# Optimization experiments

Measured on AMD Instinct MI355X. Metric: run time of the kernel, lower is better.

Reference implementation:

```python
import jax, jax.numpy as jnp
import numpy as np

EPS = 1e-5

def conv2d(x, w, b, stride, pad):
    y = jax.lax.conv_general_dilated(x, w, (stride, stride), [(pad, pad), (pad, pad)],
                                     dimension_numbers=('NCHW', 'OIHW', 'NCHW'))
    return y + b[None, :, None, None]

def group_norm(x, w, b, groups=8):
    B, C, H, W = x.shape
    xg = x.reshape(B, groups, C // groups, H, W)
    mu = xg.mean(axis=(2, 3, 4), keepdims=True)
    var = xg.var(axis=(2, 3, 4), keepdims=True)
    xn = ((xg - mu) / jnp.sqrt(var + EPS)).reshape(B, C, H, W)
    return xn * w[None, :, None, None] + b[None, :, None, None]

def _apply_1q(state, gate, wire):
    # state: (N,2,2,2,2), gate: (N,2,2) or (2,2); wire axis = wire+1
    ax = wire + 1
    st = jnp.moveaxis(state, ax, -1)
    if gate.ndim == 3:
        st = jnp.einsum('nij,n...j->n...i', gate, st)
    else:
        st = jnp.einsum('ij,n...j->n...i', gate, st)
    return jnp.moveaxis(st, -1, ax)

def _cnot(state, c, t):
    axc, axt = c + 1, t + 1
    s0 = jnp.take(state, 0, axis=axc)
    s1 = jnp.take(state, 1, axis=axc)
    axt2 = axt - 1 if axt > axc else axt
    s1 = jnp.flip(s1, axis=axt2)
    return jnp.stack([s0, s1], axis=axc)

def quanv_circuit(patches, weights):
    # patches: (N,4) angles; weights: (4,3) Rot params. Returns (N,4) <Z_i>.
    N = patches.shape[0]
    state = jnp.zeros((N, 2, 2, 2, 2), jnp.complex64).at[:, 0, 0, 0, 0].set(1.0)
    for w in range(4):
        a = patches[:, w] * 0.5
        ca, sa = jnp.cos(a), jnp.sin(a)
        # RX(angle): AngleEmbedding default rotation='X'
        rx = jnp.stack([jnp.stack([ca + 0j, -1j * sa], -1),
                        jnp.stack([-1j * sa, ca + 0j], -1)], -2)  # (N,2,2)
        phi, theta, omega = weights[w, 0], weights[w, 1], weights[w, 2]
        ct, st = jnp.cos(theta * 0.5), jnp.sin(theta * 0.5)
        # Rot(phi,theta,omega) = RZ(omega) RY(theta) RZ(phi)
        rot = jnp.stack([
            jnp.stack([jnp.exp(-1j * (phi + omega) * 0.5) * ct,
                       -jnp.exp(1j * (phi - omega) * 0.5) * st]),
            jnp.stack([jnp.exp(-1j * (phi - omega) * 0.5) * st,
                       jnp.exp(1j * (phi + omega) * 0.5) * ct])]).astype(jnp.complex64)
        gate = jnp.einsum('ij,njk->nik', rot, rx)  # fuse Rot o RX
        state = _apply_1q(state, gate, w)
    for c in range(3):
        state = _cnot(state, c, c + 1)
    probs = state.real ** 2 + state.imag ** 2  # (N,2,2,2,2)
    ez = []
    for w in range(4):
        other = tuple(ax for ax in range(1, 5) if ax != w + 1)
        p = probs.sum(axis=other)  # (N,2)
        ez.append(p[:, 0] - p[:, 1])
    return jnp.stack(ez, -1)

def _forward(x, pre_w1, pre_b1, pre_w2, pre_b2, pre_w3, pre_b3, qweights,
             conv1_w, conv1_b, gn1_w, gn1_b, conv2_w, conv2_b, gn2_w, gn2_b,
             fc1_w, fc1_b, fc2_w, fc2_b):
    h = jax.nn.relu(conv2d(x, pre_w1, pre_b1, 2, 1))
    h = jax.nn.relu(conv2d(h, pre_w2, pre_b2, 2, 1))
    h = conv2d(h, pre_w3, pre_b3, 1, 0)  # (B,4,14,14)
    B, C, H, W = h.shape
    oh, ow = H // 2, W // 2
    # torch unfold(2,2,2).unfold(3,2,2): patch flattened row-major (kh,kw)
    p = h.reshape(B, C, oh, 2, ow, 2).transpose(0, 1, 2, 4, 3, 5).reshape(B, C, oh * ow, 4)
    p = p.transpose(0, 2, 1, 3).reshape(-1, 4)
    q = quanv_circuit(p, qweights)  # (B*oh*ow*C, 4)
    q = q.reshape(B, oh * ow, C, 4).transpose(0, 2, 3, 1).reshape(B, C * 4, oh, ow)
    h = jax.nn.relu(group_norm(conv2d(q, conv1_w, conv1_b, 1, 1), gn1_w, gn1_b))
    h = jax.nn.relu(group_norm(conv2d(h, conv2_w, conv2_b, 1, 1), gn2_w, gn2_b))
    ph, pw = h.shape[2] // 2, h.shape[3] // 2
    h = h[:, :, :2 * ph, :2 * pw].reshape(B, h.shape[1], ph, 2, pw, 2).max(axis=(3, 5))
    h = h.reshape(B, -1)
    h = jax.nn.relu(h @ fc1_w.T + fc1_b)
    # dropout is identity in eval mode
    return h @ fc2_w.T + fc2_b

def setup_inputs() -> dict:
    key = jax.random.key(0)
    ks = jax.random.split(key, 16)
    def rn(k, shape, scale=0.1):
        return (jax.random.normal(k, shape) * scale).astype(jnp.float32)
    B = 1024
    return {
        'x': jax.random.uniform(ks[0], (B, 1, 64, 64), jnp.float32),
        'pre_w1': rn(ks[1], (4, 1, 3, 3)), 'pre_b1': rn(ks[1], (4,)),
        'pre_w2': rn(ks[2], (4, 4, 3, 3)), 'pre_b2': rn(ks[2], (4,)),
        'pre_w3': rn(ks[3], (4, 4, 3, 3)), 'pre_b3': rn(ks[3], (4,)),
        'qweights': jax.random.uniform(ks[4], (4, 3), jnp.float32, 0.0, 2.0 * np.pi),
        'conv1_w': rn(ks[5], (32, 16, 3, 3)), 'conv1_b': rn(ks[6], (32,)),
        'gn1_w': jnp.ones((32,), jnp.float32), 'gn1_b': jnp.zeros((32,), jnp.float32),
        'conv2_w': rn(ks[7], (64, 32, 3, 3)), 'conv2_b': rn(ks[8], (64,)),
        'gn2_w': jnp.ones((64,), jnp.float32), 'gn2_b': jnp.zeros((64,), jnp.float32),
        'fc1_w': rn(ks[9], (128, 576)), 'fc1_b': rn(ks[10], (128,)),
        'fc2_w': rn(ks[11], (10, 128)), 'fc2_b': rn(ks[12], (10,)),
    }

def reference(x, pre_w1, pre_b1, pre_w2, pre_b2, pre_w3, pre_b3, qweights,
              conv1_w, conv1_b, gn1_w, gn1_b, conv2_w, conv2_b, gn2_w, gn2_b,
              fc1_w, fc1_b, fc2_w, fc2_b):
    return _forward(x, pre_w1, pre_b1, pre_w2, pre_b2, pre_w3, pre_b3, qweights,
                    conv1_w, conv1_b, gn1_w, gn1_b, conv2_w, conv2_b, gn2_w, gn2_b,
                    fc1_w, fc1_b, fc2_w, fc2_b)
```

## Files before the change

kernel.cpp:

```cpp
#include <hip/hip_runtime.h>
#include <hip/hip_bf16.h>

#define B 1024

__global__ __launch_bounds__(256) void k_pre1(const float* __restrict__ x,
                                              const float* __restrict__ w,
                                              const float* __restrict__ bias,
                                              float* __restrict__ out,
                                              const float* __restrict__ cw1,
                                              const float* __restrict__ cw2,
                                              float* __restrict__ tw1,
                                              float* __restrict__ tw2) {
    int idx = blockIdx.x * blockDim.x + threadIdx.x;
    if (idx >= B * 32 * 32) {
        int i = idx - B * 32 * 32;
        if (i < 4608) {
            int co = i & 31; int rest = i >> 5; int k = rest % 9; int ci = rest / 9;
            tw1[i] = cw1[(co * 16 + ci) * 9 + k];
        }
        if (i < 18432) {
            int co = i & 63; int rest = i >> 6; int k = rest % 9; int ci = rest / 9;
            tw2[i] = cw2[(co * 32 + ci) * 9 + k];
        }
        return;
    }
    int b = idx >> 10;
    int rem = idx & 1023;
    int oy = rem >> 5, ox = rem & 31;
    const float* xin = x + b * 4096;
    float a0 = bias[0], a1 = bias[1], a2 = bias[2], a3 = bias[3];
#pragma unroll
    for (int ky = 0; ky < 3; ++ky) {
        int iy = 2 * oy - 1 + ky;
        if (iy < 0 || iy >= 64) continue;
#pragma unroll
        for (int kx = 0; kx < 3; ++kx) {
            int ix = 2 * ox - 1 + kx;
            if (ix < 0 || ix >= 64) continue;
            float v = xin[iy * 64 + ix];
            int k = ky * 3 + kx;
            a0 += w[k] * v;
            a1 += w[9 + k] * v;
            a2 += w[18 + k] * v;
            a3 += w[27 + k] * v;
        }
    }
    float* o = out + b * 4096 + oy * 32 + ox;
    o[0]    = fmaxf(a0, 0.f);
    o[1024] = fmaxf(a1, 0.f);
    o[2048] = fmaxf(a2, 0.f);
    o[3072] = fmaxf(a3, 0.f);
}

__global__ __launch_bounds__(256) void k_pre2(const float* __restrict__ in,
                                              const float* __restrict__ w,
                                              const float* __restrict__ bias,
                                              float* __restrict__ out) {
    int idx = blockIdx.x * blockDim.x + threadIdx.x;
    if (idx >= B * 16 * 16) return;
    int b = idx >> 8;
    int rem = idx & 255;
    int oy = rem >> 4, ox = rem & 15;
    const float* xin = in + b * 4096;
    float acc[4] = {bias[0], bias[1], bias[2], bias[3]};
#pragma unroll
    for (int ci = 0; ci < 4; ++ci) {
#pragma unroll
        for (int ky = 0; ky < 3; ++ky) {
            int iy = 2 * oy - 1 + ky;
            if (iy < 0 || iy >= 32) continue;
#pragma unroll
            for (int kx = 0; kx < 3; ++kx) {
                int ix = 2 * ox - 1 + kx;
                if (ix < 0 || ix >= 32) continue;
                float v = xin[ci * 1024 + iy * 32 + ix];
#pragma unroll
                for (int co = 0; co < 4; ++co)
                    acc[co] += w[((co * 4 + ci) * 3 + ky) * 3 + kx] * v;
            }
        }
    }
#pragma unroll
    for (int co = 0; co < 4; ++co)
        out[b * 1024 + co * 256 + oy * 16 + ox] = fmaxf(acc[co], 0.f);
}

__global__ __launch_bounds__(256) void k_pre3_quanv(const float* __restrict__ h2,
                                                    const float* __restrict__ w3,
                                                    const float* __restrict__ b3,
                                                    const float* __restrict__ qw,
                                                    float* __restrict__ q) {
    int idx = blockIdx.x * blockDim.x + threadIdx.x;
    if (idx >= B * 4 * 49) return;
    int b = idx / 196;
    int rem = idx % 196;
    int c = rem / 49;
    int pos = rem % 49;
    int oh = pos / 7, ow = pos % 7;
    const float* xin = h2 + b * 1024;
    float xv[4];
#pragma unroll
    for (int dy = 0; dy < 2; ++dy)
#pragma unroll
        for (int dx = 0; dx < 2; ++dx) {
            int oy = 2 * oh + dy, ox = 2 * ow + dx;
            float acc = b3[c];
#pragma unroll
            for (int ci = 0; ci < 4; ++ci)
#pragma unroll
                for (int ky = 0; ky < 3; ++ky)
#pragma unroll
                    for (int kx = 0; kx < 3; ++kx)
                        acc += w3[((c * 4 + ci) * 3 + ky) * 3 + kx] *
                               xin[ci * 256 + (oy + ky) * 16 + (ox + kx)];
            xv[dy * 2 + dx] = acc;
        }
    float prod = 1.f;
    float* qo = q + b * 1280 + c * 320 + 8 * (oh + 1) + ow;
#pragma unroll
    for (int w = 0; w < 4; ++w) {
        float phi = qw[w * 3 + 0];
        float theta = qw[w * 3 + 1];
        float st, ct, sx, cx;
        __sincosf(theta, &st, &ct);
        float sp = __sinf(phi);
        __sincosf(xv[w], &sx, &cx);
        float z = ct * cx - st * sp * sx;
        prod *= z;
        qo[w * 80] = prod;
    }
}

__device__ __forceinline__ void load_plane12(const float* __restrict__ p, float* dst) {
#pragma unroll
    for (int j = 0; j < 12; ++j) {
        float4 v = reinterpret_cast<const float4*>(p)[j];
        dst[4 * j] = v.x; dst[4 * j + 1] = v.y; dst[4 * j + 2] = v.z; dst[4 * j + 3] = v.w;
    }
}

template <int STRIDE>
__device__ __forceinline__ void load_w9(const float* __restrict__ p, float* w) {
#pragma unroll
    for (int k = 0; k < 9; ++k) w[k] = p[k * STRIDE];
}

__device__ __forceinline__ void conv_rows(const float* pr, const float* w9, float* acc) {
#pragma unroll
    for (int lr = 0; lr < 4; ++lr)
#pragma unroll
        for (int c = 0; c < 7; ++c)
#pragma unroll
            for (int ky = 0; ky < 3; ++ky)
#pragma unroll
                for (int kx = 0; kx < 3; ++kx) {
                    int cc = c - 1 + kx;
                    if (cc < 0) continue;
                    acc[lr * 7 + c] += w9[ky * 3 + kx] * pr[(lr + ky) * 8 + cc];
                }
}

__global__ __launch_bounds__(64, 2) void k_conv1_fused(const float* __restrict__ qb,
                                                       const float* __restrict__ tw1,
                                                       const float* __restrict__ bias,
                                                       const float* __restrict__ gw,
                                                       const float* __restrict__ gb,
                                                       float* __restrict__ g1) {
    int b = blockIdx.x;
    int lane = threadIdx.x;
    int co = lane & 31;
    int h = lane >> 5;
    const float* pin = qb + b * 1280 + 24 * h;
    float acc[28];
    float bco = bias[co];
#pragma unroll
    for (int p = 0; p < 28; ++p) acc[p] = bco;

    float pa[48], pb[48], wa[9], wb[9];
    load_plane12(pin, pa);
    load_w9<32>(tw1 + co, wa);
#pragma unroll
    for (int ci = 0; ci < 16; ci += 2) {
        load_plane12(pin + (ci + 1) * 80, pb);
        load_w9<32>(tw1 + (ci + 1) * 288 + co, wb);
        conv_rows(pa, wa, acc);
        if (ci + 2 < 16) {
            load_plane12(pin + (ci + 2) * 80, pa);
            load_w9<32>(tw1 + (ci + 2) * 288 + co, wa);
        }
        conv_rows(pb, wb, acc);
    }
    float sum = 0.f, ssq = 0.f;
#pragma unroll
    for (int lr = 0; lr < 4; ++lr) {
        float rs_ = 0.f, rq_ = 0.f;
#pragma unroll
        for (int c = 0; c < 7; ++c) { float v = acc[lr * 7 + c]; rs_ += v; rq_ += v * v; }
        if (lr > 0 || h == 0) { sum += rs_; ssq += rq_; }
    }
    sum += __shfl_xor(sum, 1);  ssq += __shfl_xor(ssq, 1);
    sum += __shfl_xor(sum, 2);  ssq += __shfl_xor(ssq, 2);
    sum += __shfl_xor(sum, 32); ssq += __shfl_xor(ssq, 32);
    float mu = sum * (1.f / 196.f);
    float var = ssq * (1.f / 196.f) - mu * mu;
    float rs = rsqrtf(var + 1e-5f);
    float ga = gw[co] * rs;
    float be = gb[co] - mu * ga;
    float* o = g1 + b * 2560 + co * 80;
#pragma unroll
    for (int lr = 0; lr < 4; ++lr) {
        if (h == 1 && lr == 0) continue;
        int row = lr + 3 * h;
        float r0 = fmaxf(acc[lr * 7 + 0] * ga + be, 0.f);
        float r1 = fmaxf(acc[lr * 7 + 1] * ga + be, 0.f);
        float r2 = fmaxf(acc[lr * 7 + 2] * ga + be, 0.f);
        float r3 = fmaxf(acc[lr * 7 + 3] * ga + be, 0.f);
        float r4 = fmaxf(acc[lr * 7 + 4] * ga + be, 0.f);
        float r5 = fmaxf(acc[lr * 7 + 5] * ga + be, 0.f);
        float r6 = fmaxf(acc[lr * 7 + 6] * ga + be, 0.f);
        float* rowp = o + 8 * (row + 1);
        *reinterpret_cast<float4*>(rowp) = make_float4(r0, r1, r2, r3);
        *reinterpret_cast<float2*>(rowp + 4) = make_float2(r4, r5);
        rowp[6] = r6;
    }
}

__global__ __launch_bounds__(64, 2) void k_conv2_fused(const float* __restrict__ g1,
                                                       const float* __restrict__ tw2,
                                                       const float* __restrict__ bias,
                                                       const float* __restrict__ gw,
                                                       const float* __restrict__ gb,
                                                       float* __restrict__ out) {
    int b = blockIdx.x >> 1;
    int wk = blockIdx.x & 1;
    int lane = threadIdx.x;
    int co = wk * 32 + (lane & 31);
    int h = lane >> 5;
    const float* pin = g1 + b * 2560 + 24 * h;
    float acc[28];
    float bco = bias[co];
#pragma unroll
    for (int p = 0; p < 28; ++p) acc[p] = bco;

    float pa[48], pb[48], wa[9], wb[9];
    load_plane12(pin, pa);
    load_w9<64>(tw2 + co, wa);
#pragma unroll
    for (int ci = 0; ci < 32; ci += 2) {
        load_plane12(pin + (ci + 1) * 80, pb);
        load_w9<64>(tw2 + (ci + 1) * 576 + co, wb);
        conv_rows(pa, wa, acc);
        if (ci + 2 < 32) {
            load_plane12(pin + (ci + 2) * 80, pa);
            load_w9<64>(tw2 + (ci + 2) * 576 + co, wa);
        }
        conv_rows(pb, wb, acc);
    }
    float sum = 0.f, ssq = 0.f;
#pragma unroll
    for (int lr = 0; lr < 4; ++lr) {
        float rs_ = 0.f, rq_ = 0.f;
#pragma unroll
        for (int c = 0; c < 7; ++c) { float v = acc[lr * 7 + c]; rs_ += v; rq_ += v * v; }
        if (lr > 0 || h == 0) { sum += rs_; ssq += rq_; }
    }
    sum += __shfl_xor(sum, 1);  ssq += __shfl_xor(ssq, 1);
    sum += __shfl_xor(sum, 2);  ssq += __shfl_xor(ssq, 2);
    sum += __shfl_xor(sum, 4);  ssq += __shfl_xor(ssq, 4);
    sum += __shfl_xor(sum, 32); ssq += __shfl_xor(ssq, 32);
    float mu = sum * (1.f / 392.f);
    float var = ssq * (1.f / 392.f) - mu * mu;
    float rs = rsqrtf(var + 1e-5f);
    float ga = gw[co] * rs;
    float be = gb[co] - mu * ga;
#pragma unroll
    for (int p = 0; p < 28; ++p) acc[p] = fmaxf(acc[p] * ga + be, 0.f);
    float* o = out + b * 576 + co * 9;
    if (h == 0) {
#pragma unroll
        for (int py = 0; py < 2; ++py)
#pragma unroll
            for (int px = 0; px < 3; ++px) {
                int p0 = (2 * py) * 7 + 2 * px;
                float m = fmaxf(fmaxf(acc[p0], acc[p0 + 1]), fmaxf(acc[p0 + 7], acc[p0 + 8]));
                o[py * 3 + px] = m;
            }
    } else {
#pragma unroll
        for (int px = 0; px < 3; ++px) {
            int p0 = 7 + 2 * px;
            float m = fmaxf(fmaxf(acc[p0], acc[p0 + 1]), fmaxf(acc[p0 + 7], acc[p0 + 8]));
            o[6 + px] = m;
        }
    }
}

__global__ __launch_bounds__(128) void k_fc(const float* __restrict__ p2,
                                            const float* __restrict__ w1,
                                            const float* __restrict__ b1,
                                            const float* __restrict__ w2,
                                            const float* __restrict__ b2,
                                            float* __restrict__ out) {
    __shared__ float s_p[8 * 576];
    __shared__ float s_f[8][132];
    int b0 = blockIdx.x * 8, tid = threadIdx.x;
    for (int i = tid; i < 8 * 576; i += 128) s_p[i] = p2[b0 * 576 + i];
    __syncthreads();
    {
        float acc[8];
        float bv = b1[tid];
#pragma unroll
        for (int s = 0; s < 8; ++s) acc[s] = bv;
        const float4* wr = reinterpret_cast<const float4*>(w1 + tid * 576);
        const float4* sp = reinterpret_cast<const float4*>(s_p);
        for (int j = 0; j < 144; ++j) {
            float4 a = wr[j];
#pragma unroll
            for (int s = 0; s < 8; ++s) {
                float4 c = sp[s * 144 + j];
                acc[s] += a.x * c.x + a.y * c.y + a.z * c.z + a.w * c.w;
            }
        }
#pragma unroll
        for (int s = 0; s < 8; ++s) s_f[s][tid] = fmaxf(acc[s], 0.f);
    }
    __syncthreads();
    if (tid < 80) {
        int s = tid / 10, o = tid % 10;
        float acc = b2[o];
        const float* wr = w2 + o * 128;
#pragma unroll 8
        for (int j = 0; j < 128; ++j) acc += wr[j] * s_f[s][j];
        out[(b0 + s) * 10 + o] = acc;
    }
}

extern "C" void kernel_launch(void* const* d_in, const int* in_sizes, int n_in,
                              void* d_out, int out_size, void* d_ws, size_t ws_size,
                              hipStream_t stream) {
    const float* x       = (const float*)d_in[0];
    const float* pre_w1  = (const float*)d_in[1];
    const float* pre_b1  = (const float*)d_in[2];
    const float* pre_w2  = (const float*)d_in[3];
    const float* pre_b2  = (const float*)d_in[4];
    const float* pre_w3  = (const float*)d_in[5];
    const float* pre_b3  = (const float*)d_in[6];
    const float* qweights= (const float*)d_in[7];
    const float* conv1_w = (const float*)d_in[8];
    const float* conv1_b = (const float*)d_in[9];
    const float* gn1_w   = (const float*)d_in[10];
    const float* gn1_b   = (const float*)d_in[11];
    const float* conv2_w = (const float*)d_in[12];
    const float* conv2_b = (const float*)d_in[13];
    const float* gn2_w   = (const float*)d_in[14];
    const float* gn2_b   = (const float*)d_in[15];
    const float* fc1_w   = (const float*)d_in[16];
    const float* fc1_b   = (const float*)d_in[17];
    const float* fc2_w   = (const float*)d_in[18];
    const float* fc2_b   = (const float*)d_in[19];
    float* out = (float*)d_out;

    float* ws = (float*)d_ws;
    float* h1 = ws;
    float* qb = ws;
    float* g1 = ws + 1310720;
    float* h2 = ws + 4194304;
    float* p2 = ws + 4194304;
    float* tw1 = ws + 6045696;
    float* tw2 = ws + 6045696 + 4608;

    k_pre1<<<4168, 256, 0, stream>>>(x, pre_w1, pre_b1, h1, conv1_w, conv2_w, tw1, tw2);
    k_pre2<<<(B * 16 * 16 + 255) / 256, 256, 0, stream>>>(h1, pre_w2, pre_b2, h2);
    hipMemsetAsync(ws, 0, 3932160 * sizeof(float), stream);
    k_pre3_quanv<<<(B * 4 * 49 + 255) / 256, 256, 0, stream>>>(h2, pre_w3, pre_b3, qweights, qb);
    k_conv1_fused<<<B, 64, 0, stream>>>(qb, tw1, conv1_b, gn1_w, gn1_b, g1);
    k_conv2_fused<<<2 * B, 64, 0, stream>>>(g1, tw2, conv2_b, gn2_w, gn2_b, p2);
    k_fc<<<(B / 8), 128, 0, stream>>>(p2, fc1_w, fc1_b, fc2_w, fc2_b, out);
}
```

Baseline: 215.3 us.

## Fuse conv1 and conv2 kernels through shared-memory intermediate

```diff
diff --git a/kernel.cpp b/kernel.cpp
--- a/kernel.cpp
+++ b/kernel.cpp
@@ -160,98 +160,101 @@
                 }
 }
 
-__global__ __launch_bounds__(64, 2) void k_conv1_fused(const float* __restrict__ qb,
-                                                       const float* __restrict__ tw1,
-                                                       const float* __restrict__ bias,
-                                                       const float* __restrict__ gw,
-                                                       const float* __restrict__ gb,
-                                                       float* __restrict__ g1) {
+__global__ __launch_bounds__(128, 2) void k_conv12_fused(const float* __restrict__ qb,
+                                                         const float* __restrict__ tw1,
+                                                         const float* __restrict__ b1,
+                                                         const float* __restrict__ gw1,
+                                                         const float* __restrict__ gb1,
+                                                         const float* __restrict__ tw2,
+                                                         const float* __restrict__ b2c,
+                                                         const float* __restrict__ gw2,
+                                                         const float* __restrict__ gb2,
+                                                         float* __restrict__ out) {
+    __shared__ float s_g1[32 * 84];
     int b = blockIdx.x;
-    int lane = threadIdx.x;
-    int co = lane & 31;
+    int wave = threadIdx.x >> 6;
+    int lane = threadIdx.x & 63;
+    int col = lane & 31;
     int h = lane >> 5;
-    const float* pin = qb + b * 1280 + 24 * h;
+
+    if (wave == 0) {
+        const float* pin = qb + b * 1280 + 24 * h;
+        float acc[28];
+        float bco = b1[col];
+#pragma unroll
+        for (int p = 0; p < 28; ++p) acc[p] = bco;
+        float pa[48], pb[48], wa[9], wb[9];
+        load_plane12(pin, pa);
+        load_w9<32>(tw1 + col, wa);
+#pragma unroll
+        for (int ci = 0; ci < 16; ci += 2) {
+            load_plane12(pin + (ci + 1) * 80, pb);
+            load_w9<32>(tw1 + (ci + 1) * 288 + col, wb);
+            conv_rows(pa, wa, acc);
+            if (ci + 2 < 16) {
+                load_plane12(pin + (ci + 2) * 80, pa);
+                load_w9<32>(tw1 + (ci + 2) * 288 + col, wa);
+            }
+            conv_rows(pb, wb, acc);
+        }
+        float sum = 0.f, ssq = 0.f;
+#pragma unroll
+        for (int lr = 0; lr < 4; ++lr) {
+            float rs_ = 0.f, rq_ = 0.f;
+#pragma unroll
+            for (int c = 0; c < 7; ++c) { float v = acc[lr * 7 + c]; rs_ += v; rq_ += v * v; }
+            if (lr > 0 || h == 0) { sum += rs_; ssq += rq_; }
+        }
+        sum += __shfl_xor(sum, 1);  ssq += __shfl_xor(ssq, 1);
+        sum += __shfl_xor(sum, 2);  ssq += __shfl_xor(ssq, 2);
+        sum += __shfl_xor(sum, 32); ssq += __shfl_xor(ssq, 32);
+        float mu = sum * (1.f / 196.f);
+        float var = ssq * (1.f / 196.f) - mu * mu;
+        float rs = rsqrtf(var + 1e-5f);
+        float ga = gw1[col] * rs;
+        float be = gb1[col] - mu * ga;
+        float* o = s_g1 + col * 84;
+        if (h == 0) {
+            *reinterpret_cast<float4*>(o)     = make_float4(0.f, 0.f, 0.f, 0.f);
+            *reinterpret_cast<float4*>(o + 4) = make_float4(0.f, 0.f, 0.f, 0.f);
+        } else {
+            *reinterpret_cast<float4*>(o + 64) = make_float4(0.f, 0.f, 0.f, 0.f);
+            *reinterpret_cast<float4*>(o + 68) = make_float4(0.f, 0.f, 0.f, 0.f);
+        }
+#pragma unroll
+        for (int lr = 0; lr < 4; ++lr) {
+            if (h == 1 && lr == 0) continue;
+            int row = lr + 3 * h;
+            float r0 = fmaxf(acc[lr * 7 + 0] * ga + be, 0.f);
+            float r1 = fmaxf(acc[lr * 7 + 1] * ga + be, 0.f);
+            float r2 = fmaxf(acc[lr * 7 + 2] * ga + be, 0.f);
+            float r3 = fmaxf(acc[lr * 7 + 3] * ga + be, 0.f);
+            float r4 = fmaxf(acc[lr * 7 + 4] * ga + be, 0.f);
+            float r5 = fmaxf(acc[lr * 7 + 5] * ga + be, 0.f);
+            float r6 = fmaxf(acc[lr * 7 + 6] * ga + be, 0.f);
+            float* rowp = o + 8 * (row + 1);
+            *reinterpret_cast<float4*>(rowp)     = make_float4(r0, r1, r2, r3);
+            *reinterpret_cast<float4*>(rowp + 4) = make_float4(r4, r5, r6, 0.f);
+        }
+    }
+    __syncthreads();
+
+    int co = wave * 32 + col;
+    const float* pin = s_g1 + 24 * h;
     float acc[28];
-    float bco = bias[co];
+    float bco = b2c[co];
 #pragma unroll
     for (int p = 0; p < 28; ++p) acc[p] = bco;
-
-    float pa[48], pb[48], wa[9], wb[9];
-    load_plane12(pin, pa);
-    load_w9<32>(tw1 + co, wa);
-#pragma unroll
-    for (int ci = 0; ci < 16; ci += 2) {
-        load_plane12(pin + (ci + 1) * 80, pb);
-        load_w9<32>(tw1 + (ci + 1) * 288 + co, wb);
-        conv_rows(pa, wa, acc);
-        if (ci + 2 < 16) {
-            load_plane12(pin + (ci + 2) * 80, pa);
-            load_w9<32>(tw1 + (ci + 2) * 288 + co, wa);
-        }
-        conv_rows(pb, wb, acc);
-    }
-    float sum = 0.f, ssq = 0.f;
-#pragma unroll
-    for (int lr = 0; lr < 4; ++lr) {
-        float rs_ = 0.f, rq_ = 0.f;
-#pragma unroll
-        for (int c = 0; c < 7; ++c) { float v = acc[lr * 7 + c]; rs_ += v; rq_ += v * v; }
-        if (lr > 0 || h == 0) { sum += rs_; ssq += rq_; }
-    }
-    sum += __shfl_xor(sum, 1);  ssq += __shfl_xor(ssq, 1);
-    sum += __shfl_xor(sum, 2);  ssq += __shfl_xor(ssq, 2);
-    sum += __shfl_xor(sum, 32); ssq += __shfl_xor(ssq, 32);
-    float mu = sum * (1.f / 196.f);
-    float var = ssq * (1.f / 196.f) - mu * mu;
-    float rs = rsqrtf(var + 1e-5f);
-    float ga = gw[co] * rs;
-    float be = gb[co] - mu * ga;
-    float* o = g1 + b * 2560 + co * 80;
-#pragma unroll
-    for (int lr = 0; lr < 4; ++lr) {
-        if (h == 1 && lr == 0) continue;
-        int row = lr + 3 * h;
-        float r0 = fmaxf(acc[lr * 7 + 0] * ga + be, 0.f);
-        float r1 = fmaxf(acc[lr * 7 + 1] * ga + be, 0.f);
-        float r2 = fmaxf(acc[lr * 7 + 2] * ga + be, 0.f);
-        float r3 = fmaxf(acc[lr * 7 + 3] * ga + be, 0.f);
-        float r4 = fmaxf(acc[lr * 7 + 4] * ga + be, 0.f);
-        float r5 = fmaxf(acc[lr * 7 + 5] * ga + be, 0.f);
-        float r6 = fmaxf(acc[lr * 7 + 6] * ga + be, 0.f);
-        float* rowp = o + 8 * (row + 1);
-        *reinterpret_cast<float4*>(rowp) = make_float4(r0, r1, r2, r3);
-        *reinterpret_cast<float2*>(rowp + 4) = make_float2(r4, r5);
-        rowp[6] = r6;
-    }
-}
-
-__global__ __launch_bounds__(64, 2) void k_conv2_fused(const float* __restrict__ g1,
-                                                       const float* __restrict__ tw2,
-                                                       const float* __restrict__ bias,
-                                                       const float* __restrict__ gw,
-                                                       const float* __restrict__ gb,
-                                                       float* __restrict__ out) {
-    int b = blockIdx.x >> 1;
-    int wk = blockIdx.x & 1;
-    int lane = threadIdx.x;
-    int co = wk * 32 + (lane & 31);
-    int h = lane >> 5;
-    const float* pin = g1 + b * 2560 + 24 * h;
-    float acc[28];
-    float bco = bias[co];
-#pragma unroll
-    for (int p = 0; p < 28; ++p) acc[p] = bco;
-
     float pa[48], pb[48], wa[9], wb[9];
     load_plane12(pin, pa);
     load_w9<64>(tw2 + co, wa);
 #pragma unroll
     for (int ci = 0; ci < 32; ci += 2) {
-        load_plane12(pin + (ci + 1) * 80, pb);
+        load_plane12(pin + (ci + 1) * 84, pb);
         load_w9<64>(tw2 + (ci + 1) * 576 + co, wb);
         conv_rows(pa, wa, acc);
         if (ci + 2 < 32) {
-            load_plane12(pin + (ci + 2) * 80, pa);
+            load_plane12(pin + (ci + 2) * 84, pa);
             load_w9<64>(tw2 + (ci + 2) * 576 + co, wa);
         }
         conv_rows(pb, wb, acc);
@@ -271,8 +274,8 @@
     float mu = sum * (1.f / 392.f);
     float var = ssq * (1.f / 392.f) - mu * mu;
     float rs = rsqrtf(var + 1e-5f);
-    float ga = gw[co] * rs;
-    float be = gb[co] - mu * ga;
+    float ga = gw2[co] * rs;
+    float be = gb2[co] - mu * ga;
 #pragma unroll
     for (int p = 0; p < 28; ++p) acc[p] = fmaxf(acc[p] * ga + be, 0.f);
     float* o = out + b * 576 + co * 9;
@@ -363,7 +366,6 @@
     float* ws = (float*)d_ws;
     float* h1 = ws;
     float* qb = ws;
-    float* g1 = ws + 1310720;
     float* h2 = ws + 4194304;
     float* p2 = ws + 4194304;
     float* tw1 = ws + 6045696;
@@ -371,9 +373,9 @@
 
     k_pre1<<<4168, 256, 0, stream>>>(x, pre_w1, pre_b1, h1, conv1_w, conv2_w, tw1, tw2);
     k_pre2<<<(B * 16 * 16 + 255) / 256, 256, 0, stream>>>(h1, pre_w2, pre_b2, h2);
-    hipMemsetAsync(ws, 0, 3932160 * sizeof(float), stream);
+    hipMemsetAsync(ws, 0, 1310720 * sizeof(float), stream);
     k_pre3_quanv<<<(B * 4 * 49 + 255) / 256, 256, 0, stream>>>(h2, pre_w3, pre_b3, qweights, qb);
-    k_conv1_fused<<<B, 64, 0, stream>>>(qb, tw1, conv1_b, gn1_w, gn1_b, g1);
-    k_conv2_fused<<<2 * B, 64, 0, stream>>>(g1, tw2, conv2_b, gn2_w, gn2_b, p2);
+    k_conv12_fused<<<B, 128, 0, stream>>>(qb, tw1, conv1_b, gn1_w, gn1_b,
+                                          tw2, conv2_b, gn2_w, gn2_b, p2);
     k_fc<<<(B / 8), 128, 0, stream>>>(p2, fc1_w, fc1_b, fc2_w, fc2_b, out);
 }
```

Result: faster. 199.8 us (-7.2%).
